# Performance work log

Measured on AMD Instinct MI355X. Metric: run time of the kernel, lower is better.

## Reference

```python
import jax, jax.numpy as jnp
import numpy as np

K = 10
SLOPE = 0.2
FEATS = [3, 64, 128, 256, 512, 1024]
MLP = [1024, 128, 64, 1]
B, N = 8, 2048


def setup_inputs() -> dict:
    key = jax.random.key(0)
    keys = jax.random.split(key, 32)
    inp = {"x": jax.random.normal(keys[0], (B, N, 3), dtype=jnp.float32)}
    ki = 1
    for i in range(5):
        fin, fout = 2 * FEATS[i], FEATS[i + 1]
        s = 1.0 / np.sqrt(fin)
        inp[f"w{i}"] = jax.random.uniform(keys[ki], (fin, fout), jnp.float32, -s, s); ki += 1
        inp[f"b{i}"] = jax.random.uniform(keys[ki], (fout,), jnp.float32, -s, s); ki += 1
    for i in range(3):
        fin, fout = MLP[i], MLP[i + 1]
        s = 1.0 / np.sqrt(fin)
        inp[f"m{i}w"] = jax.random.uniform(keys[ki], (fin, fout), jnp.float32, -s, s); ki += 1
        inp[f"m{i}b"] = jax.random.uniform(keys[ki], (fout,), jnp.float32, -s, s); ki += 1
    return inp


def _knn_idx(xb):
    # xb: [N, F]; squared euclidean distances, self included (dist 0)
    sq = jnp.sum(xb * xb, axis=-1)
    d2 = sq[:, None] + sq[None, :] - 2.0 * (xb @ xb.T)
    _, idx = jax.lax.top_k(-d2, K)  # [N, K] nearest (incl. self)
    return idx


def _edge_conv(x, W, b):
    # x: [B, N, F] -> [B, N, Fout]
    fin = x.shape[-1]
    W1, W2 = W[:fin], W[fin:]  # split concat([x_i, x_j - x_i]) @ W
    idx = jax.vmap(_knn_idx)(x)  # [B, N, K]
    x_j = jax.vmap(lambda xb, ib: xb[ib])(x, idx)  # [B, N, K, F]
    h_center = x @ W1 + b  # [B, N, Fout]
    diff = x_j - x[:, :, None, :]
    h = h_center[:, :, None, :] + jnp.einsum('bnkf,fo->bnko', diff, W2)
    h = jnp.where(h > 0, h, SLOPE * h)  # LeakyReLU(0.2)
    return jnp.max(h, axis=2)  # max aggregation over neighbors


def reference(x, w0, b0, w1, b1, w2, b2, w3, b3, w4, b4,
              m0w, m0b, m1w, m1b, m2w, m2b):
    ws = [(w0, b0), (w1, b1), (w2, b2), (w3, b3), (w4, b4)]
    h = x
    for W, b in ws:
        h = _edge_conv(h, W, b)
    g = jnp.max(h, axis=1)  # MaxPool1d(kernel=2048) -> global max over points: [B, 1024]
    g = g @ m0w + m0b
    g = g @ m1w + m1b
    g = g @ m2w + m2b
    return g  # [B, 1]
```

## Files before the change

### kernel.cpp

```cpp
#include <hip/hip_runtime.h>
#include <hip/hip_bf16.h>
#include <math.h>

#define BB 8
#define NN 2048
#define KK 10
#define BN (BB * NN)
#define HC 1024
#define GCH 64

typedef __attribute__((ext_vector_type(8))) short bf16x8;
typedef __attribute__((ext_vector_type(4))) float f32x4;

__device__ inline unsigned short f2bf(float f) {
    unsigned int u = __float_as_uint(f);
    unsigned int r = u + 0x7fffu + ((u >> 16) & 1u);
    return (unsigned short)(r >> 16);
}
__device__ inline float bf2f(unsigned short h) {
    return __uint_as_float((unsigned int)h << 16);
}

__device__ __forceinline__ void async16(const void* g, void* l) {
    __builtin_amdgcn_global_load_lds(
        (const __attribute__((address_space(1))) void*)g,
        (__attribute__((address_space(3))) void*)l, 16, 0, 0);
}

__global__ void xsplit3_kernel(const float* __restrict__ x,
                               unsigned short* __restrict__ hi,
                               unsigned short* __restrict__ lo,
                               float* __restrict__ sq) {
    int row = blockIdx.x * blockDim.x + threadIdx.x;
    if (row >= BN) return;
    unsigned short hbuf[32], lbuf[32];
#pragma unroll
    for (int f = 0; f < 32; ++f) { hbuf[f] = 0; lbuf[f] = 0; }
    float s = 0.f;
#pragma unroll
    for (int f = 0; f < 3; ++f) {
        float v = x[(size_t)row * 3 + f];
        s += v * v;
        unsigned short h = f2bf(v);
        hbuf[f] = h;
        lbuf[f] = f2bf(v - bf2f(h));
    }
    sq[row] = s;
#pragma unroll
    for (int f = 0; f < 32; f += 8) {
        *(uint4*)&hi[(size_t)row * 32 + f] = *(uint4*)&hbuf[f];
        *(uint4*)&lo[(size_t)row * 32 + f] = *(uint4*)&lbuf[f];
    }
}

__global__ void wsplit_all_kernel(const float* __restrict__ w0, const float* __restrict__ w1,
                                  const float* __restrict__ w2, const float* __restrict__ w3,
                                  const float* __restrict__ w4, unsigned short* __restrict__ WTall) {
    const int fins[5]  = {3, 64, 128, 256, 512};
    const int fpads[5] = {32, 64, 128, 256, 512};
    const int fouts[5] = {64, 128, 256, 512, 1024};
    const int eoff[6]  = {0, 4096, 20480, 86016, 348160, 1396736};
    const int woff[5]  = {0, 8192, 40960, 172032, 696320};
    int i = blockIdx.x * blockDim.x + threadIdx.x;
    if (i >= 1396736) return;
    int l;
    if (i < eoff[1]) l = 0; else if (i < eoff[2]) l = 1;
    else if (i < eoff[3]) l = 2; else if (i < eoff[4]) l = 3; else l = 4;
    int e = i - eoff[l];
    const float* w = (l == 0) ? w0 : (l == 1) ? w1 : (l == 2) ? w2 : (l == 3) ? w3 : w4;
    int fin = fins[l], fpad = fpads[l], fout = fouts[l];
    unsigned short* WT = WTall + woff[l];
    int op = e % (2 * fout);
    int f = e / (2 * fout);
    float v = 0.f;
    if (f < fin) {
        if (op < fout) v = w[(size_t)f * fout + op] - w[(size_t)(fin + f) * fout + op];
        else v = w[(size_t)(fin + f) * fout + (op - fout)];
    }
    unsigned short h = f2bf(v);
    unsigned short lo = f2bf(v - bf2f(h));
    WT[(size_t)op * (2 * fpad) + f] = h;
    WT[(size_t)op * (2 * fpad) + fpad + f] = lo;
}

__global__ __launch_bounds__(256) void knn_gram_kernel(
        const unsigned short* __restrict__ xh, const unsigned short* __restrict__ xl,
        const float* __restrict__ sq, float* __restrict__ d2a,
        float* __restrict__ d2b, int F) {
    int b = blockIdx.y;
    int t = blockIdx.x, ti = 0;
    while (t >= 16 - ti) { t -= 16 - ti; ti++; }
    int tj = ti + t;
    int row0 = ti * 128;
    int col0 = tj * 128;
    const unsigned short* xhb = xh + (size_t)b * NN * F;
    const unsigned short* xlb = xl + (size_t)b * NN * F;
    const float* sqb = sq + (size_t)b * NN;

    __shared__ __align__(16) unsigned char smem_raw[33024];
    unsigned short* Ah = (unsigned short*)smem_raw;
    unsigned short* Al = Ah + 128 * 32;
    unsigned short* Bh = Al + 128 * 32;
    unsigned short* Bl = Bh + 128 * 32;
    float* LT = (float*)smem_raw;

    int tid = threadIdx.x;
    int lane = tid & 63;
    int wave = tid >> 6;
    int wr = (wave >> 1) * 64, wc = (wave & 1) * 64;
    int l15 = lane & 15, kq = lane >> 4;
    int rsub = lane >> 2;
    int csub = (((lane & 3) ^ ((lane >> 3) & 3))) * 8;
    int kqs = (kq ^ ((l15 >> 1) & 3)) * 8;

    f32x4 acc[4][4];
#pragma unroll
    for (int mt = 0; mt < 4; ++mt)
#pragma unroll
        for (int nt = 0; nt < 4; ++nt) acc[mt][nt] = (f32x4){0.f, 0.f, 0.f, 0.f};

    for (int kc = 0; kc < F; kc += 32) {
        __syncthreads();
#pragma unroll
        for (int j = 0; j < 2; ++j) {
            int row = wave * 32 + j * 16 + rsub;
            int dsto = wave * 1024 + j * 512;
            async16(xhb + (size_t)(row0 + row) * F + kc + csub, Ah + dsto);
            async16(xlb + (size_t)(row0 + row) * F + kc + csub, Al + dsto);
            async16(xhb + (size_t)(col0 + row) * F + kc + csub, Bh + dsto);
            async16(xlb + (size_t)(col0 + row) * F + kc + csub, Bl + dsto);
        }
        __syncthreads();
        bf16x8 bh[4], bl[4];
#pragma unroll
        for (int t4 = 0; t4 < 4; ++t4) {
            bh[t4] = *(const bf16x8*)&Bh[(wc + t4 * 16 + l15) * 32 + kqs];
            bl[t4] = *(const bf16x8*)&Bl[(wc + t4 * 16 + l15) * 32 + kqs];
        }
#pragma unroll
        for (int mt = 0; mt < 4; ++mt) {
            bf16x8 ah = *(const bf16x8*)&Ah[(wr + mt * 16 + l15) * 32 + kqs];
            bf16x8 al = *(const bf16x8*)&Al[(wr + mt * 16 + l15) * 32 + kqs];
#pragma unroll
            for (int nt = 0; nt < 4; ++nt) {
                acc[mt][nt] = __builtin_amdgcn_mfma_f32_16x16x32_bf16(ah, bh[nt], acc[mt][nt], 0, 0, 0);
                acc[mt][nt] = __builtin_amdgcn_mfma_f32_16x16x32_bf16(al, bh[nt], acc[mt][nt], 0, 0, 0);
                acc[mt][nt] = __builtin_amdgcn_mfma_f32_16x16x32_bf16(ah, bl[nt], acc[mt][nt], 0, 0, 0);
            }
        }
    }
    {
        float* dst = (col0 < HC) ? d2a : d2b;
        int lc0 = col0 & (HC - 1);
#pragma unroll
        for (int mt = 0; mt < 4; ++mt) {
            int rbase = row0 + wr + mt * 16 + kq * 4;
#pragma unroll
            for (int nt = 0; nt < 4; ++nt) {
                int cc = wc + nt * 16 + l15;
                float sqc = sqb[col0 + cc];
#pragma unroll
                for (int r = 0; r < 4; ++r) {
                    float v = (sqb[rbase + r] + sqc) - 2.f * acc[mt][nt][r];
                    acc[mt][nt][r] = v;
                    dst[((size_t)b * NN + rbase + r) * HC + lc0 + cc] = v;
                }
            }
        }
    }
    if (ti != tj) {
        float* mdst = (row0 < HC) ? d2a : d2b;
        int mc0 = row0 & (HC - 1);
#pragma unroll
        for (int h = 0; h < 2; ++h) {
            __syncthreads();
            if ((wave & 1) == h) {
#pragma unroll
                for (int mt = 0; mt < 4; ++mt)
#pragma unroll
                    for (int nt = 0; nt < 4; ++nt)
#pragma unroll
                        for (int r = 0; r < 4; ++r)
                            LT[(nt * 16 + l15) * 129 + (wr + mt * 16 + kq * 4 + r)] =
                                acc[mt][nt][r];
            }
            __syncthreads();
#pragma unroll
            for (int it = 0; it < 8; ++it) {
                int v = tid + it * 256;
                int lr = v >> 5, c4 = v & 31;
                float4 val;
                val.x = LT[lr * 129 + c4 * 4];
                val.y = LT[lr * 129 + c4 * 4 + 1];
                val.z = LT[lr * 129 + c4 * 4 + 2];
                val.w = LT[lr * 129 + c4 * 4 + 3];
                *(float4*)&mdst[((size_t)b * NN + col0 + h * 64 + lr) * HC + mc0 + c4 * 4] = val;
            }
        }
    }
}

__global__ __launch_bounds__(256) void knn_select_kernel(
        const float* __restrict__ d2a, const float* __restrict__ d2b,
        int* __restrict__ idx) {
    int row = blockIdx.x * 4 + (threadIdx.x >> 6);
    int lane = threadIdx.x & 63;
    const float* ra = d2a + (size_t)row * HC;
    const float* rb = d2b + (size_t)row * HC;

    float4 v[8];
#pragma unroll
    for (int it = 0; it < 4; ++it) {
        v[it]     = *(const float4*)&ra[it * 256 + lane * 4];
        v[it + 4] = *(const float4*)&rb[it * 256 + lane * 4];
    }

    float bestd[KK];
    int besti[KK];
#pragma unroll
    for (int k = 0; k < KK; ++k) { bestd[k] = INFINITY; besti[k] = 0x7fffffff; }

#pragma unroll
    for (int it = 0; it < 8; ++it) {
        int cbase = ((it < 4) ? (it * 256) : (HC + (it - 4) * 256)) + lane * 4;
        float dv[4] = {v[it].x, v[it].y, v[it].z, v[it].w};
#pragma unroll
        for (int s4 = 0; s4 < 4; ++s4) {
            float d = dv[s4];
            if (d < bestd[KK - 1]) {
                bestd[KK - 1] = d;
                besti[KK - 1] = cbase + s4;
#pragma unroll
                for (int s = KK - 1; s > 0; --s) {
                    if (bestd[s] < bestd[s - 1]) {
                        float td = bestd[s]; bestd[s] = bestd[s - 1]; bestd[s - 1] = td;
                        int ti = besti[s]; besti[s] = besti[s - 1]; besti[s - 1] = ti;
                    }
                }
            }
        }
    }

    int h = 0;
    int mywin = 0;
    for (int s = 0; s < KK; ++s) {
        float dd = (h < KK) ? bestd[h] : INFINITY;
        int ii = (h < KK) ? besti[h] : 0x7fffffff;
        float d0 = dd; int i0 = ii;
#pragma unroll
        for (int off = 32; off > 0; off >>= 1) {
            float od = __shfl_xor(dd, off);
            int oi = __shfl_xor(ii, off);
            if (od < dd || (od == dd && oi < ii)) { dd = od; ii = oi; }
        }
        if (lane == s) mywin = ii;
        if (h < KK && i0 == ii && d0 == dd) h++;
    }
    if (lane < KK) idx[(size_t)row * KK + lane] = mywin;
}

__global__ __launch_bounds__(256) void gemm2_mfma_kernel(
        const unsigned short* __restrict__ XSh, const unsigned short* __restrict__ XSl,
        const unsigned short* __restrict__ WT, const float* __restrict__ bias,
        float* __restrict__ Aout, float* __restrict__ Tout, int fin, int fout) {
    int m0 = blockIdx.x * 128;
    int n0 = blockIdx.y * 128;
    __shared__ __align__(16) unsigned short AsB[4 * 128 * 32];
    unsigned short* Ah = AsB;
    unsigned short* Al = Ah + 128 * 32;
    unsigned short* Bh = Al + 128 * 32;
    unsigned short* Bl = Bh + 128 * 32;

    int tid = threadIdx.x;
    int lane = tid & 63;
    int wave = tid >> 6;
    int wr = (wave >> 1) * 64, wc = (wave & 1) * 64;
    int l15 = lane & 15, kq = lane >> 4;
    int rsub = lane >> 2;
    int csub = (((lane & 3) ^ ((lane >> 3) & 3))) * 8;
    int kqs = (kq ^ ((l15 >> 1) & 3)) * 8;
    int w2f = 2 * fin;

    f32x4 acc[4][4];
#pragma unroll
    for (int mt = 0; mt < 4; ++mt)
#pragma unroll
        for (int nt = 0; nt < 4; ++nt) acc[mt][nt] = (f32x4){0.f, 0.f, 0.f, 0.f};

    for (int kc = 0; kc < fin; kc += 32) {
        __syncthreads();
#pragma unroll
        for (int j = 0; j < 2; ++j) {
            int row = wave * 32 + j * 16 + rsub;
            int dsto = wave * 1024 + j * 512;
            async16(XSh + (size_t)(m0 + row) * fin + kc + csub, Ah + dsto);
            async16(XSl + (size_t)(m0 + row) * fin + kc + csub, Al + dsto);
            async16(WT + (size_t)(n0 + row) * w2f + kc + csub, Bh + dsto);
            async16(WT + (size_t)(n0 + row) * w2f + fin + kc + csub, Bl + dsto);
        }
        __syncthreads();
        bf16x8 bh[4], bl[4];
#pragma unroll
        for (int t = 0; t < 4; ++t) {
            bh[t] = *(const bf16x8*)&Bh[(wc + t * 16 + l15) * 32 + kqs];
            bl[t] = *(const bf16x8*)&Bl[(wc + t * 16 + l15) * 32 + kqs];
        }
#pragma unroll
        for (int mt = 0; mt < 4; ++mt) {
            bf16x8 ah = *(const bf16x8*)&Ah[(wr + mt * 16 + l15) * 32 + kqs];
            bf16x8 al = *(const bf16x8*)&Al[(wr + mt * 16 + l15) * 32 + kqs];
#pragma unroll
            for (int nt = 0; nt < 4; ++nt) {
                acc[mt][nt] = __builtin_amdgcn_mfma_f32_16x16x32_bf16(ah, bh[nt], acc[mt][nt], 0, 0, 0);
                acc[mt][nt] = __builtin_amdgcn_mfma_f32_16x16x32_bf16(al, bh[nt], acc[mt][nt], 0, 0, 0);
                acc[mt][nt] = __builtin_amdgcn_mfma_f32_16x16x32_bf16(ah, bl[nt], acc[mt][nt], 0, 0, 0);
            }
        }
    }
#pragma unroll
    for (int mt = 0; mt < 4; ++mt) {
        int mbase = m0 + wr + mt * 16 + kq * 4;
#pragma unroll
        for (int nt = 0; nt < 4; ++nt) {
            int oc = n0 + wc + nt * 16 + l15;
            f32x4 c = acc[mt][nt];
            if (oc < fout) {
                float bv = bias[oc];
#pragma unroll
                for (int r = 0; r < 4; ++r)
                    Aout[(size_t)(mbase + r) * fout + oc] = c[r] + bv;
            } else {
                int o2 = oc - fout;
#pragma unroll
                for (int r = 0; r < 4; ++r)
                    Tout[(size_t)(mbase + r) * fout + o2] = c[r];
            }
        }
    }
}

__device__ __forceinline__ const unsigned short* tbaseA(
        const unsigned short* XSh, const unsigned short* XSl, int F, int t) {
    int ko = t * 64;
    if (ko < F) return XSh + ko;
    if (ko < 2 * F) return XSl + (ko - F);
    return XSh + (ko - 2 * F);
}
__device__ __forceinline__ const unsigned short* tbaseB(
        const unsigned short* WT, int F, int t) {
    int ko = t * 64;
    if (ko < F) return WT + ko;
    if (ko < 2 * F) return WT + (ko - F);
    return WT + F + (ko - 2 * F);
}

#define GBAR() asm volatile("s_barrier" ::: "memory")

__global__ __launch_bounds__(512, 2) void gemm2_8ph_kernel(
        const unsigned short* __restrict__ XSh, const unsigned short* __restrict__ XSl,
        const unsigned short* __restrict__ WT, const float* __restrict__ bias,
        float* __restrict__ Aout, float* __restrict__ Tout, int F, int fout, int nby) {
    __shared__ __align__(16) unsigned short Lds[65536];

    int nwg = gridDim.x;
    int bid = blockIdx.x;
    int q = nwg >> 3;
    int swz = (bid & 7) * q + (bid >> 3);
    int by = swz % nby;
    int bx = swz / nby;
    int m0 = bx * 256, n0 = by * 256;

    int tid = threadIdx.x;
    int lane = tid & 63;
    int wave = tid >> 6;
    int mw = wave >> 2;
    int nw = wave & 3;
    int l15 = lane & 15, kq = lane >> 4;
    int rx7 = l15 & 7;

    int isA = (wave < 4);
    size_t rowmul = isA ? (size_t)F : (size_t)(2 * F);
    int orgn = isA ? m0 : n0;
    int r8 = lane >> 3;
    int cb8 = ((lane & 7) ^ r8) * 8;
    int subb = (wave & 3) * 8;
    int ldsoA = isA ? 0 : 16384;

    int nt = (3 * F) >> 6;

    f32x4 acc[8][4];
#pragma unroll
    for (int mt = 0; mt < 8; ++mt)
#pragma unroll
        for (int nn = 0; nn < 4; ++nn) acc[mt][nn] = (f32x4){0.f, 0.f, 0.f, 0.f};

    auto stage = [&](const unsigned short* tb, int par, int j) {
        int sub = subb + j;
        async16(tb + (size_t)(orgn + sub * 8 + r8) * rowmul + cb8,
                Lds + par * 32768 + ldsoA + sub * 512);
    };

    {
        const unsigned short* t0 = isA ? tbaseA(XSh, XSl, F, 0) : tbaseB(WT, F, 0);
        const unsigned short* t1 = isA ? tbaseA(XSh, XSl, F, 1) : tbaseB(WT, F, 1);
#pragma unroll
        for (int j = 0; j < 8; ++j) stage(t0, 0, j);
#pragma unroll
        for (int j = 0; j < 4; ++j) stage(t1, 1, j);
    }
    asm volatile("s_waitcnt vmcnt(4)" ::: "memory");
    GBAR();

    for (int t = 0; t < nt; ++t) {
        const unsigned short* Ab = Lds + (t & 1) * 32768;
        const unsigned short* Bb = Ab + 16384;
        bool s1 = (t + 1 < nt), s2 = (t + 2 < nt);
        const unsigned short* tb1 = s1 ? (isA ? tbaseA(XSh, XSl, F, t + 1)
                                              : tbaseB(WT, F, t + 1)) : XSh;
        const unsigned short* tb2 = s2 ? (isA ? tbaseA(XSh, XSl, F, t + 2)
                                              : tbaseB(WT, F, t + 2)) : XSh;
        int p1 = (t + 1) & 1, p0 = t & 1;

        bf16x8 aF[4][2], bA[2][2], bB[2][2];

#pragma unroll
        for (int mt = 0; mt < 4; ++mt)
#pragma unroll
            for (int kf = 0; kf < 2; ++kf)
                aF[mt][kf] = *(const bf16x8*)&Ab[(mw * 128 + mt * 16 + l15) * 64 +
                                                 ((kf * 4 + kq) ^ rx7) * 8];
#pragma unroll
        for (int nn = 0; nn < 2; ++nn)
#pragma unroll
            for (int kf = 0; kf < 2; ++kf)
                bA[nn][kf] = *(const bf16x8*)&Bb[(nw * 64 + nn * 16 + l15) * 64 +
                                                 ((kf * 4 + kq) ^ rx7) * 8];
        if (s1) { stage(tb1, p1, 4); stage(tb1, p1, 5); }
        GBAR();
        __builtin_amdgcn_s_setprio(1);
#pragma unroll
        for (int mt = 0; mt < 4; ++mt)
#pragma unroll
            for (int nn = 0; nn < 2; ++nn) {
                acc[mt][nn] = __builtin_amdgcn_mfma_f32_16x16x32_bf16(aF[mt][0], bA[nn][0], acc[mt][nn], 0, 0, 0);
                acc[mt][nn] = __builtin_amdgcn_mfma_f32_16x16x32_bf16(aF[mt][1], bA[nn][1], acc[mt][nn], 0, 0, 0);
            }
        __builtin_amdgcn_s_setprio(0);
        GBAR();

#pragma unroll
        for (int nn = 0; nn < 2; ++nn)
#pragma unroll
            for (int kf = 0; kf < 2; ++kf)
                bB[nn][kf] = *(const bf16x8*)&Bb[(nw * 64 + (nn + 2) * 16 + l15) * 64 +
                                                 ((kf * 4 + kq) ^ rx7) * 8];
        if (s1) { stage(tb1, p1, 6); stage(tb1, p1, 7); }
        GBAR();
        __builtin_amdgcn_s_setprio(1);
#pragma unroll
        for (int mt = 0; mt < 4; ++mt)
#pragma unroll
            for (int nn = 0; nn < 2; ++nn) {
                acc[mt][nn + 2] = __builtin_amdgcn_mfma_f32_16x16x32_bf16(aF[mt][0], bB[nn][0], acc[mt][nn + 2], 0, 0, 0);
                acc[mt][nn + 2] = __builtin_amdgcn_mfma_f32_16x16x32_bf16(aF[mt][1], bB[nn][1], acc[mt][nn + 2], 0, 0, 0);
            }
        __builtin_amdgcn_s_setprio(0);
        GBAR();

#pragma unroll
        for (int mt = 0; mt < 4; ++mt)
#pragma unroll
            for (int kf = 0; kf < 2; ++kf)
                aF[mt][kf] = *(const bf16x8*)&Ab[(mw * 128 + (mt + 4) * 16 + l15) * 64 +
                                                 ((kf * 4 + kq) ^ rx7) * 8];
        GBAR();
        __builtin_amdgcn_s_setprio(1);
#pragma unroll
        for (int mt = 0; mt < 4; ++mt)
#pragma unroll
            for (int nn = 0; nn < 2; ++nn) {
                acc[mt + 4][nn] = __builtin_amdgcn_mfma_f32_16x16x32_bf16(aF[mt][0], bA[nn][0], acc[mt + 4][nn], 0, 0, 0);
                acc[mt + 4][nn] = __builtin_amdgcn_mfma_f32_16x16x32_bf16(aF[mt][1], bA[nn][1], acc[mt + 4][nn], 0, 0, 0);
            }
        __builtin_amdgcn_s_setprio(0);
        GBAR();

        if (s2) { stage(tb2, p0, 0); stage(tb2, p0, 1); stage(tb2, p0, 2); stage(tb2, p0, 3); }
        GBAR();
        __builtin_amdgcn_s_setprio(1);
#pragma unroll
        for (int mt = 0; mt < 4; ++mt)
#pragma unroll
            for (int nn = 0; nn < 2; ++nn) {
                acc[mt + 4][nn + 2] = __builtin_amdgcn_mfma_f32_16x16x32_bf16(aF[mt][0], bB[nn][0], acc[mt + 4][nn + 2], 0, 0, 0);
                acc[mt + 4][nn + 2] = __builtin_amdgcn_mfma_f32_16x16x32_bf16(aF[mt][1], bB[nn][1], acc[mt + 4][nn + 2], 0, 0, 0);
            }
        __builtin_amdgcn_s_setprio(0);
        if (s2)      asm volatile("s_waitcnt vmcnt(4)" ::: "memory");
        else if (s1) asm volatile("s_waitcnt vmcnt(0)" ::: "memory");
        GBAR();
    }

#pragma unroll
    for (int mt = 0; mt < 8; ++mt) {
        int mbase = m0 + mw * 128 + mt * 16 + kq * 4;
#pragma unroll
        for (int nn = 0; nn < 4; ++nn) {
            int oc = n0 + nw * 64 + nn * 16 + l15;
            f32x4 c = acc[mt][nn];
            if (oc < fout) {
                float bv = bias[oc];
#pragma unroll
                for (int r = 0; r < 4; ++r)
                    Aout[(size_t)(mbase + r) * fout + oc] = c[r] + bv;
            } else {
                int o2 = oc - fout;
#pragma unroll
                for (int r = 0; r < 4; ++r)
                    Tout[(size_t)(mbase + r) * fout + o2] = c[r];
            }
        }
    }
}

__global__ __launch_bounds__(256) void gathermax_fused_kernel(
        const float* __restrict__ A, const float* __restrict__ T,
        const int* __restrict__ idx, unsigned short* __restrict__ hi,
        unsigned short* __restrict__ lo, float* __restrict__ sq, int shift) {
    int b = blockIdx.y;
    int wave = threadIdx.x >> 6;
    int lane = threadIdx.x & 63;
    int pnl = blockIdx.x * 4 + wave;
    int pn = (b << 11) + pnl;
    int fout = 1 << shift;
    int nf4 = fout >> 2;
    const float* Tb = T + ((size_t)b << 11) * fout;
    const int* ip = idx + (size_t)pn * KK;
    int j[KK];
#pragma unroll
    for (int k = 0; k < KK; ++k) j[k] = ip[k];

    float s = 0.f;
    for (int f4 = lane; f4 < nf4; f4 += 64) {
        int o = f4 * 4;
        float4 m = {-INFINITY, -INFINITY, -INFINITY, -INFINITY};
#pragma unroll
        for (int k = 0; k < KK; ++k) {
            float4 t = *(const float4*)&Tb[(size_t)j[k] * fout + o];
            m.x = fmaxf(m.x, t.x); m.y = fmaxf(m.y, t.y);
            m.z = fmaxf(m.z, t.z); m.w = fmaxf(m.w, t.w);
        }
        float4 a = *(const float4*)&A[(size_t)pn * fout + o];
        float h4[4];
        h4[0] = a.x + m.x; h4[1] = a.y + m.y; h4[2] = a.z + m.z; h4[3] = a.w + m.w;
        uint2 uh, ul;
        unsigned short hs[4], ls[4];
#pragma unroll
        for (int q = 0; q < 4; ++q) {
            float h = h4[q] > 0.f ? h4[q] : 0.2f * h4[q];
            s += h * h;
            unsigned short hh = f2bf(h);
            hs[q] = hh;
            ls[q] = f2bf(h - bf2f(hh));
        }
        uh.x = (unsigned)hs[0] | ((unsigned)hs[1] << 16);
        uh.y = (unsigned)hs[2] | ((unsigned)hs[3] << 16);
        ul.x = (unsigned)ls[0] | ((unsigned)ls[1] << 16);
        ul.y = (unsigned)ls[2] | ((unsigned)ls[3] << 16);
        *(uint2*)&hi[(size_t)pn * fout + o] = uh;
        *(uint2*)&lo[(size_t)pn * fout + o] = ul;
    }
#pragma unroll
    for (int off = 32; off > 0; off >>= 1) s += __shfl_down(s, off);
    if (lane == 0) sq[pn] = s;
}

__global__ __launch_bounds__(256) void gathermax_gmax_kernel(
        const float* __restrict__ A, const float* __restrict__ T,
        const int* __restrict__ idx, float* __restrict__ gp) {
    int chunk = blockIdx.x;
    int b = blockIdx.y;
    int o = threadIdx.x * 4;
    const float* Tb = T + ((size_t)b << 11) * 1024;
    float4 gm = {-INFINITY, -INFINITY, -INFINITY, -INFINITY};
    for (int p = 0; p < NN / GCH; ++p) {
        int pnl = chunk * (NN / GCH) + p;
        int pn = (b << 11) + pnl;
        const int* ip = idx + (size_t)pn * KK;
        float4 m = {-INFINITY, -INFINITY, -INFINITY, -INFINITY};
#pragma unroll
        for (int k = 0; k < KK; ++k) {
            int j = ip[k];
            float4 t = *(const float4*)&Tb[(size_t)j * 1024 + o];
            m.x = fmaxf(m.x, t.x); m.y = fmaxf(m.y, t.y);
            m.z = fmaxf(m.z, t.z); m.w = fmaxf(m.w, t.w);
        }
        float4 a = *(const float4*)&A[(size_t)pn * 1024 + o];
        float4 h;
        h.x = a.x + m.x; h.y = a.y + m.y; h.z = a.z + m.z; h.w = a.w + m.w;
        h.x = h.x > 0.f ? h.x : 0.2f * h.x;
        h.y = h.y > 0.f ? h.y : 0.2f * h.y;
        h.z = h.z > 0.f ? h.z : 0.2f * h.z;
        h.w = h.w > 0.f ? h.w : 0.2f * h.w;
        gm.x = fmaxf(gm.x, h.x); gm.y = fmaxf(gm.y, h.y);
        gm.z = fmaxf(gm.z, h.z); gm.w = fmaxf(gm.w, h.w);
    }
    *(float4*)&gp[((size_t)chunk * BB + b) * 1024 + o] = gm;
}

__global__ void gmax2_kernel(const float* __restrict__ gp, float* __restrict__ g) {
    int i = blockIdx.x * 256 + threadIdx.x;
    int b = i >> 10, o = i & 1023;
    float m = -INFINITY;
    for (int c = 0; c < GCH; ++c) m = fmaxf(m, gp[((size_t)c * BB + b) * 1024 + o]);
    g[(size_t)b * 1024 + o] = m;
}

__global__ __launch_bounds__(256) void mlp1_kernel(
        const float* __restrict__ g, const float* __restrict__ m0w,
        const float* __restrict__ m0b, float* __restrict__ H1) {
    int wid = blockIdx.x * 4 + (threadIdx.x >> 6);
    int lane = threadIdx.x & 63;
    int b = wid >> 7, t = wid & 127;
    float s = 0.f;
    for (int f = lane; f < 1024; f += 64)
        s += g[(size_t)b * 1024 + f] * m0w[(size_t)f * 128 + t];
#pragma unroll
    for (int off = 32; off > 0; off >>= 1) s += __shfl_down(s, off);
    if (lane == 0) H1[(size_t)b * 128 + t] = s + m0b[t];
}

__global__ __launch_bounds__(256) void mlp2_kernel(
        const float* __restrict__ H1, const float* __restrict__ m1w,
        const float* __restrict__ m1b, float* __restrict__ H2) {
    int wid = blockIdx.x * 4 + (threadIdx.x >> 6);
    int lane = threadIdx.x & 63;
    int b = wid >> 6, t = wid & 63;
    float s = 0.f;
    for (int f = lane; f < 128; f += 64)
        s += H1[(size_t)b * 128 + f] * m1w[(size_t)f * 64 + t];
#pragma unroll
    for (int off = 32; off > 0; off >>= 1) s += __shfl_down(s, off);
    if (lane == 0) H2[(size_t)b * 64 + t] = s + m1b[t];
}

__global__ __launch_bounds__(256) void mlp3_kernel(
        const float* __restrict__ H2, const float* __restrict__ m2w,
        const float* __restrict__ m2b, float* __restrict__ out) {
    int b = blockIdx.x * 4 + (threadIdx.x >> 6);
    int lane = threadIdx.x & 63;
    if (b >= BB) return;
    float s = H2[(size_t)b * 64 + lane] * m2w[lane];
#pragma unroll
    for (int off = 32; off > 0; off >>= 1) s += __shfl_down(s, off);
    if (lane == 0) out[b] = s + m2b[0];
}

extern "C" void kernel_launch(void* const* d_in, const int* in_sizes, int n_in,
                              void* d_out, int out_size, void* d_ws, size_t ws_size,
                              hipStream_t stream) {
    const float* x0 = (const float*)d_in[0];
    const float* w[5], * bi[5];
    for (int i = 0; i < 5; ++i) { w[i] = (const float*)d_in[1 + 2 * i]; bi[i] = (const float*)d_in[2 + 2 * i]; }
    const float* m0w = (const float*)d_in[11]; const float* m0b = (const float*)d_in[12];
    const float* m1w = (const float*)d_in[13]; const float* m1b = (const float*)d_in[14];
    const float* m2w = (const float*)d_in[15]; const float* m2b = (const float*)d_in[16];

    const int fouts[5] = {64, 128, 256, 512, 1024};
    const int shifts[5] = {6, 7, 8, 9, 10};
    const int woff[5] = {0, 8192, 40960, 172032, 696320};
    const size_t WTALL = 2793472;

    float* X0 = (float*)d_ws;
    float* X1 = X0 + (size_t)BN * 1024;
    float* T  = X1 + (size_t)BN * 1024;
    float* SQ = T  + (size_t)BN * 1024;
    int*   IDX = (int*)(SQ + BN);
    unsigned short* XSh = (unsigned short*)(IDX + (size_t)BN * KK);
    unsigned short* XSl = XSh + (size_t)BN * 512;
    unsigned short* WTall = XSl + (size_t)BN * 512;
    float* GP = (float*)(WTall + WTALL);
    float* G  = GP + (size_t)GCH * BB * 1024;
    float* H1 = G + (size_t)BB * 1024;
    float* H2 = H1 + (size_t)BB * 128;
    float* bufs[2] = {X0, X1};

    xsplit3_kernel<<<(BN + 255) / 256, 256, 0, stream>>>(x0, XSh, XSl, SQ);
    wsplit_all_kernel<<<(1396736 + 255) / 256, 256, 0, stream>>>(w[0], w[1], w[2], w[3], w[4], WTall);

    int fin = 3;
    for (int l = 0; l < 5; ++l) {
        int fout = fouts[l];
        float* nxt = bufs[l & 1];
        int Fg = (l == 0) ? 32 : fin;

        dim3 gg2(136, BB);
        knn_gram_kernel<<<gg2, 256, 0, stream>>>(XSh, XSl, SQ, T, nxt, Fg);
        knn_select_kernel<<<BN / 4, 256, 0, stream>>>(T, nxt, IDX);

        if (l == 3) {
            int nby = (2 * fout) / 256;
            gemm2_8ph_kernel<<<dim3(64 * nby), 512, 0, stream>>>(
                XSh, XSl, WTall + woff[l], bi[l], nxt, T, fin, fout, nby);
        } else {
            dim3 gg(BN / 128, (2 * fout) / 128);
            gemm2_mfma_kernel<<<gg, 256, 0, stream>>>(XSh, XSl, WTall + woff[l], bi[l], nxt, T, Fg, fout);
        }

        if (l < 4) {
            dim3 gmg(NN / 4, BB);
            gathermax_fused_kernel<<<gmg, 256, 0, stream>>>(nxt, T, IDX, XSh, XSl, SQ, shifts[l]);
        } else {
            dim3 gmg(GCH, BB);
            gathermax_gmax_kernel<<<gmg, 256, 0, stream>>>(nxt, T, IDX, GP);
        }

        fin = fout;
    }

    gmax2_kernel<<<32, 256, 0, stream>>>(GP, G);
    mlp1_kernel<<<256, 256, 0, stream>>>(G, m0w, m0b, H1);
    mlp2_kernel<<<128, 256, 0, stream>>>(H1, m1w, m1b, H2);
    mlp3_kernel<<<2, 256, 0, stream>>>(H2, m2w, m2b, (float*)d_out);
}
```

Before: 1.006 ms.

## Fuse per-tile top-K selection into gram kernel and merge candidates per row

The gram kernel no longer writes the full pairwise distance matrix. It computes a per-row top-10 for each 128x128 tile inside the kernel, including the mirrored tile, and writes compact (distance, index) candidates, 16 tiles by 10 per point. A new merge kernel reduces those 160 candidates per row to the final 10 with a wave-level merge. The aim is to remove the large global write and read-back of the distance matrix at every layer. In exchange, the gram kernel now runs serial insertion sorts on only some of its threads, which may underuse the compute units.

```diff
diff --git a/kernel.cpp b/kernel.cpp
--- a/kernel.cpp
+++ b/kernel.cpp
@@ -6,8 +6,8 @@
 #define NN 2048
 #define KK 10
 #define BN (BB * NN)
-#define HC 1024
 #define GCH 64
+#define NTILE 16
 
 typedef __attribute__((ext_vector_type(8))) short bf16x8;
 typedef __attribute__((ext_vector_type(4))) float f32x4;
@@ -85,8 +85,7 @@
 
 __global__ __launch_bounds__(256) void knn_gram_kernel(
         const unsigned short* __restrict__ xh, const unsigned short* __restrict__ xl,
-        const float* __restrict__ sq, float* __restrict__ d2a,
-        float* __restrict__ d2b, int F) {
+        const float* __restrict__ sq, float2* __restrict__ cand, int F) {
     int b = blockIdx.y;
     int t = blockIdx.x, ti = 0;
     while (t >= 16 - ti) { t -= 16 - ti; ti++; }
@@ -149,103 +148,116 @@
             }
         }
     }
-    {
-        float* dst = (col0 < HC) ? d2a : d2b;
-        int lc0 = col0 & (HC - 1);
-#pragma unroll
-        for (int mt = 0; mt < 4; ++mt) {
-            int rbase = row0 + wr + mt * 16 + kq * 4;
-#pragma unroll
-            for (int nt = 0; nt < 4; ++nt) {
-                int cc = wc + nt * 16 + l15;
-                float sqc = sqb[col0 + cc];
-#pragma unroll
-                for (int r = 0; r < 4; ++r) {
-                    float v = (sqb[rbase + r] + sqc) - 2.f * acc[mt][nt][r];
-                    acc[mt][nt][r] = v;
-                    dst[((size_t)b * NN + rbase + r) * HC + lc0 + cc] = v;
+
+#pragma unroll
+    for (int mt = 0; mt < 4; ++mt) {
+        int rbase = row0 + wr + mt * 16 + kq * 4;
+#pragma unroll
+        for (int nt = 0; nt < 4; ++nt) {
+            int cc = wc + nt * 16 + l15;
+            float sqc = sqb[col0 + cc];
+#pragma unroll
+            for (int r = 0; r < 4; ++r)
+                acc[mt][nt][r] = (sqb[rbase + r] + sqc) - 2.f * acc[mt][nt][r];
+        }
+    }
+
+    float dD[KK]; int iD[KK];
+    if (tid < 128) {
+#pragma unroll
+        for (int k = 0; k < KK; ++k) { dD[k] = INFINITY; iD[k] = 0x7fffffff; }
+    }
+#pragma unroll
+    for (int h = 0; h < 2; ++h) {
+        __syncthreads();
+        if ((wave & 1) == h) {
+#pragma unroll
+            for (int mt = 0; mt < 4; ++mt)
+#pragma unroll
+                for (int nt = 0; nt < 4; ++nt)
+#pragma unroll
+                    for (int r = 0; r < 4; ++r)
+                        LT[(nt * 16 + l15) * 129 + (wr + mt * 16 + kq * 4 + r)] =
+                            acc[mt][nt][r];
+        }
+        __syncthreads();
+        if (tid < 128) {
+            int row = tid;
+            int cb = col0 + h * 64;
+#pragma unroll 8
+            for (int c = 0; c < 64; ++c) {
+                float d = LT[c * 129 + row];
+                if (d < dD[KK - 1]) {
+                    dD[KK - 1] = d; iD[KK - 1] = cb + c;
+#pragma unroll
+                    for (int s = KK - 1; s > 0; --s)
+                        if (dD[s] < dD[s - 1]) {
+                            float td = dD[s]; dD[s] = dD[s - 1]; dD[s - 1] = td;
+                            int tx = iD[s]; iD[s] = iD[s - 1]; iD[s - 1] = tx;
+                        }
                 }
             }
-        }
-    }
-    if (ti != tj) {
-        float* mdst = (row0 < HC) ? d2a : d2b;
-        int mc0 = row0 & (HC - 1);
-#pragma unroll
-        for (int h = 0; h < 2; ++h) {
-            __syncthreads();
-            if ((wave & 1) == h) {
-#pragma unroll
-                for (int mt = 0; mt < 4; ++mt)
-#pragma unroll
-                    for (int nt = 0; nt < 4; ++nt)
-#pragma unroll
-                        for (int r = 0; r < 4; ++r)
-                            LT[(nt * 16 + l15) * 129 + (wr + mt * 16 + kq * 4 + r)] =
-                                acc[mt][nt][r];
-            }
-            __syncthreads();
-#pragma unroll
-            for (int it = 0; it < 8; ++it) {
-                int v = tid + it * 256;
-                int lr = v >> 5, c4 = v & 31;
-                float4 val;
-                val.x = LT[lr * 129 + c4 * 4];
-                val.y = LT[lr * 129 + c4 * 4 + 1];
-                val.z = LT[lr * 129 + c4 * 4 + 2];
-                val.w = LT[lr * 129 + c4 * 4 + 3];
-                *(float4*)&mdst[((size_t)b * NN + col0 + h * 64 + lr) * HC + mc0 + c4 * 4] = val;
-            }
-        }
-    }
-}
-
-__global__ __launch_bounds__(256) void knn_select_kernel(
-        const float* __restrict__ d2a, const float* __restrict__ d2b,
-        int* __restrict__ idx) {
+        } else if (tid < 192 && ti != tj) {
+            int cq = tid - 128;
+            float dM[KK]; int iM[KK];
+#pragma unroll
+            for (int k = 0; k < KK; ++k) { dM[k] = INFINITY; iM[k] = 0x7fffffff; }
+#pragma unroll 8
+            for (int r = 0; r < 128; ++r) {
+                float d = LT[cq * 129 + r];
+                if (d < dM[KK - 1]) {
+                    dM[KK - 1] = d; iM[KK - 1] = row0 + r;
+#pragma unroll
+                    for (int s = KK - 1; s > 0; --s)
+                        if (dM[s] < dM[s - 1]) {
+                            float td = dM[s]; dM[s] = dM[s - 1]; dM[s - 1] = td;
+                            int tx = iM[s]; iM[s] = iM[s - 1]; iM[s - 1] = tx;
+                        }
+                }
+            }
+            float2* cw = cand + ((size_t)b * NN + col0 + h * 64 + cq) * (NTILE * KK)
+                              + ti * KK;
+#pragma unroll
+            for (int k = 0; k < KK; ++k)
+                cw[k] = make_float2(dM[k], __int_as_float(iM[k]));
+        }
+    }
+    if (tid < 128) {
+        float2* cw = cand + ((size_t)b * NN + row0 + tid) * (NTILE * KK)
+                          + tj * KK;
+#pragma unroll
+        for (int k = 0; k < KK; ++k)
+            cw[k] = make_float2(dD[k], __int_as_float(iD[k]));
+    }
+}
+
+__global__ __launch_bounds__(256) void knn_merge_kernel(
+        const float2* __restrict__ cand, int* __restrict__ idx) {
     int row = blockIdx.x * 4 + (threadIdx.x >> 6);
     int lane = threadIdx.x & 63;
-    const float* ra = d2a + (size_t)row * HC;
-    const float* rb = d2b + (size_t)row * HC;
-
-    float4 v[8];
-#pragma unroll
-    for (int it = 0; it < 4; ++it) {
-        v[it]     = *(const float4*)&ra[it * 256 + lane * 4];
-        v[it + 4] = *(const float4*)&rb[it * 256 + lane * 4];
-    }
-
-    float bestd[KK];
-    int besti[KK];
-#pragma unroll
-    for (int k = 0; k < KK; ++k) { bestd[k] = INFINITY; besti[k] = 0x7fffffff; }
-
-#pragma unroll
-    for (int it = 0; it < 8; ++it) {
-        int cbase = ((it < 4) ? (it * 256) : (HC + (it - 4) * 256)) + lane * 4;
-        float dv[4] = {v[it].x, v[it].y, v[it].z, v[it].w};
-#pragma unroll
-        for (int s4 = 0; s4 < 4; ++s4) {
-            float d = dv[s4];
-            if (d < bestd[KK - 1]) {
-                bestd[KK - 1] = d;
-                besti[KK - 1] = cbase + s4;
-#pragma unroll
-                for (int s = KK - 1; s > 0; --s) {
-                    if (bestd[s] < bestd[s - 1]) {
-                        float td = bestd[s]; bestd[s] = bestd[s - 1]; bestd[s - 1] = td;
-                        int ti = besti[s]; besti[s] = besti[s - 1]; besti[s - 1] = ti;
-                    }
-                }
-            }
-        }
-    }
+    const float2* cp = cand + (size_t)row * (NTILE * KK);
+
+    float d[3]; int ix[3];
+    float2 e0 = cp[lane];
+    float2 e1 = cp[lane + 64];
+    d[0] = e0.x; ix[0] = __float_as_int(e0.y);
+    d[1] = e1.x; ix[1] = __float_as_int(e1.y);
+    if (lane < 32) {
+        float2 e2 = cp[lane + 128];
+        d[2] = e2.x; ix[2] = __float_as_int(e2.y);
+    } else { d[2] = INFINITY; ix[2] = 0x7fffffff; }
+
+#define CSW(a, b) if (d[b] < d[a] || (d[b] == d[a] && ix[b] < ix[a])) { \
+        float td = d[a]; d[a] = d[b]; d[b] = td; \
+        int tx = ix[a]; ix[a] = ix[b]; ix[b] = tx; }
+    CSW(0, 1) CSW(1, 2) CSW(0, 1)
+#undef CSW
 
     int h = 0;
     int mywin = 0;
     for (int s = 0; s < KK; ++s) {
-        float dd = (h < KK) ? bestd[h] : INFINITY;
-        int ii = (h < KK) ? besti[h] : 0x7fffffff;
+        float dd = (h < 3) ? d[h] : INFINITY;
+        int ii = (h < 3) ? ix[h] : 0x7fffffff;
         float d0 = dd; int i0 = ii;
 #pragma unroll
         for (int off = 32; off > 0; off >>= 1) {
@@ -254,7 +266,7 @@
             if (od < dd || (od == dd && oi < ii)) { dd = od; ii = oi; }
         }
         if (lane == s) mywin = ii;
-        if (h < KK && i0 == ii && d0 == dd) h++;
+        if (h < 3 && i0 == ii && d0 == dd) h++;
     }
     if (lane < KK) idx[(size_t)row * KK + lane] = mywin;
 }
@@ -684,6 +696,7 @@
     float* H1 = G + (size_t)BB * 1024;
     float* H2 = H1 + (size_t)BB * 128;
     float* bufs[2] = {X0, X1};
+    float2* CAND = (float2*)T;
 
     xsplit3_kernel<<<(BN + 255) / 256, 256, 0, stream>>>(x0, XSh, XSl, SQ);
     wsplit_all_kernel<<<(1396736 + 255) / 256, 256, 0, stream>>>(w[0], w[1], w[2], w[3], w[4], WTall);
@@ -695,8 +708,8 @@
         int Fg = (l == 0) ? 32 : fin;
 
         dim3 gg2(136, BB);
-        knn_gram_kernel<<<gg2, 256, 0, stream>>>(XSh, XSl, SQ, T, nxt, Fg);
-        knn_select_kernel<<<BN / 4, 256, 0, stream>>>(T, nxt, IDX);
+        knn_gram_kernel<<<gg2, 256, 0, stream>>>(XSh, XSl, SQ, CAND, Fg);
+        knn_merge_kernel<<<BN / 4, 256, 0, stream>>>(CAND, IDX);
 
         if (l == 3) {
             int nby = (2 * fout) / 256;
```

New measurement: 1.325 ms. +31.7%, slower.
